# Optimization experiments

Measured on AMD Instinct MI355X. Metric: run time of the kernel, lower is better.

Reference implementation:

```python
import jax, jax.numpy as jnp
import numpy as np

BATCH, N_IN, N_OUT = 1024, 512, 512
GRID, DEGREE = 8, 3
NUM_BASIS = GRID + DEGREE  # 11
LO, HI = -3.0, 3.0
_h = (HI - LO) / GRID
# extended knot vector: GRID + 2*DEGREE + 1 knots -> GRID + DEGREE basis functions
KNOTS = jnp.asarray(np.linspace(LO - DEGREE * _h, HI + DEGREE * _h,
                                GRID + 2 * DEGREE + 1), dtype=jnp.float32)


def bspline_basis(x):
    """Cox-de Boor recursion. x: (batch, n_in) -> (batch, n_in, NUM_BASIS)."""
    t = KNOTS
    xb = x[..., None]
    B = ((xb >= t[:-1]) & (xb < t[1:])).astype(x.dtype)  # degree 0
    for d in range(1, DEGREE + 1):
        left = (xb - t[:-(d + 1)]) / (t[d:-1] - t[:-(d + 1)])
        right = (t[d + 1:] - xb) / (t[d + 1:] - t[1:-d])
        B = left * B[..., :-1] + right * B[..., 1:]
    return B


def setup_inputs() -> dict:
    key = jax.random.key(0)
    kx, kc, kw = jax.random.split(key, 3)
    x = jax.random.normal(kx, (BATCH, N_IN), dtype=jnp.float32)
    # xavier_normal_ init for c: fan_in = num_basis, fan_out = n_in*n_out
    c_std = float(np.sqrt(2.0 / (N_IN * N_OUT + NUM_BASIS)))
    c = jax.random.normal(kc, (N_IN * N_OUT, NUM_BASIS), dtype=jnp.float32) * c_std
    w_std = float(np.sqrt(2.0 / (N_IN + N_OUT)))
    w = jax.random.normal(kw, (N_IN, N_OUT), dtype=jnp.float32) * w_std
    return {"x": x, "c": c, "w": w}


def reference(x, c, w):
    # spline basis: (batch, n_in, K)
    bx = bspline_basis(x)
    # per-edge coefficients: (n_in, n_out, K)
    cr = c.reshape(N_IN, N_OUT, NUM_BASIS)
    # out[b,i,o] = sum_k bx[b,i,k] * c[i,o,k]
    spline = jnp.einsum('bik,iok->bio', bx, cr)
    # w * (silu(x) + spline), summed over n_in -> (batch, n_out)
    out = jnp.einsum('io,bio->bo', w, jax.nn.silu(x)[..., None] + spline)
    return out
```

## Files before the change

### kernel.cpp

```cpp
#include <hip/hip_runtime.h>

#define BATCH 1024
#define NIN   512
#define NOUT  512
#define NB    11
#define KSPLINE (NIN * NB)
#define KDIM    (KSPLINE + NIN)
#define SPLITS  8
#define BK      32

typedef short bf16x8 __attribute__((ext_vector_type(8)));
typedef float f32x4  __attribute__((ext_vector_type(4)));

__device__ __forceinline__ unsigned short f2bf(float f) {
  unsigned u = __float_as_uint(f);
  u += 0x7fff + ((u >> 16) & 1);
  return (unsigned short)(u >> 16);
}

__global__ __launch_bounds__(256) void k_basis(const float* __restrict__ x,
                                               unsigned short* __restrict__ A) {
  int tid = blockIdx.x * 256 + threadIdx.x;
  float xv = x[tid];
  float B[14];
#pragma unroll
  for (int j = 0; j < 14; ++j) {
    float t0 = -5.25f + 0.75f * (float)j;
    float t1 = t0 + 0.75f;
    B[j] = (xv >= t0 && xv < t1) ? 1.0f : 0.0f;
  }
#pragma unroll
  for (int d = 1; d <= 3; ++d) {
    float inv = 1.0f / (0.75f * (float)d);
#pragma unroll
    for (int j = 0; j <= 13 - d; ++j) {
      float tj   = -5.25f + 0.75f * (float)j;
      float tjd1 = tj + 0.75f * (float)(d + 1);
      B[j] = (xv - tj) * inv * B[j] + (tjd1 - xv) * inv * B[j + 1];
    }
  }
  int b = tid >> 9, i = tid & 511;
  unsigned short* row = A + (size_t)b * KDIM;
#pragma unroll
  for (int j = 0; j < NB; ++j) row[i * NB + j] = f2bf(B[j]);
  float sig = 1.0f / (1.0f + __expf(-xv));
  row[KSPLINE + i] = f2bf(xv * sig);
}

__global__ __launch_bounds__(256) void k_coef(const float* __restrict__ c,
                                              const float* __restrict__ w,
                                              unsigned short* __restrict__ Bt) {
  int o  = blockIdx.x;
  int kk = blockIdx.y * 256 + threadIdx.x;
  float v;
  if (kk < KSPLINE) {
    int i = kk / NB;
    int k = kk - i * NB;
    v = c[(size_t)(i * NOUT + o) * NB + k] * w[i * NOUT + o];
  } else {
    int i = kk - KSPLINE;
    v = w[i * NOUT + o];
  }
  Bt[(size_t)o * KDIM + kk] = f2bf(v);
}

__global__ __launch_bounds__(256) void k_gemm(const unsigned short* __restrict__ A,
                                              const unsigned short* __restrict__ Bt,
                                              float* __restrict__ out,
                                              int kchunk) {
  __shared__ unsigned short As[128 * BK];
  __shared__ unsigned short Bs[128 * BK];
  const int tid  = threadIdx.x;
  const int lane = tid & 63, wave = tid >> 6;
  const int wr = wave >> 1, wc = wave & 1;
  const int mbase = blockIdx.x * 128, nbase = blockIdx.y * 128;
  const int split = blockIdx.z;
  const int k0 = split * kchunk;

  f32x4 acc[4][4] = {};

  const int mrow = lane & 15;
  const int kq   = (lane >> 4) * 8;

  for (int kk = k0; kk < k0 + kchunk; kk += BK) {
#pragma unroll
    for (int it = 0; it < 2; ++it) {
      int ch  = it * 256 + tid;
      int row = ch >> 2, col = (ch & 3) * 8;
      const unsigned short* ga = A  + (size_t)(mbase + row) * KDIM + kk + col;
      const unsigned short* gb = Bt + (size_t)(nbase + row) * KDIM + kk + col;
      unsigned short* la = As + (it * 256 + wave * 64) * 8;
      unsigned short* lb = Bs + (it * 256 + wave * 64) * 8;
      __builtin_amdgcn_global_load_lds((__attribute__((address_space(1))) const void*)ga,
                                       (__attribute__((address_space(3))) void*)la, 16, 0, 0);
      __builtin_amdgcn_global_load_lds((__attribute__((address_space(1))) const void*)gb,
                                       (__attribute__((address_space(3))) void*)lb, 16, 0, 0);
    }
    __syncthreads();

    bf16x8 af[4], bfr[4];
#pragma unroll
    for (int mt = 0; mt < 4; ++mt)
      af[mt] = *(const bf16x8*)&As[(wr * 64 + mt * 16 + mrow) * BK + kq];
#pragma unroll
    for (int nt = 0; nt < 4; ++nt)
      bfr[nt] = *(const bf16x8*)&Bs[(wc * 64 + nt * 16 + mrow) * BK + kq];
#pragma unroll
    for (int mt = 0; mt < 4; ++mt)
#pragma unroll
      for (int nt = 0; nt < 4; ++nt)
        acc[mt][nt] = __builtin_amdgcn_mfma_f32_16x16x32_bf16(af[mt], bfr[nt], acc[mt][nt], 0, 0, 0);
    __syncthreads();
  }

  const int rq = (lane >> 4) * 4;
#pragma unroll
  for (int mt = 0; mt < 4; ++mt)
#pragma unroll
    for (int nt = 0; nt < 4; ++nt) {
      int colg = nbase + wc * 64 + nt * 16 + mrow;
#pragma unroll
      for (int r = 0; r < 4; ++r) {
        int rowg = mbase + wr * 64 + mt * 16 + rq + r;
        out[((size_t)split * BATCH + rowg) * NOUT + colg] = acc[mt][nt][r];
      }
    }
}

__global__ __launch_bounds__(256) void k_reduce(const float* __restrict__ part,
                                                float* __restrict__ out) {
  int t = blockIdx.x * 256 + threadIdx.x;
  f32x4 s = ((const f32x4*)part)[t];
#pragma unroll
  for (int sp = 1; sp < SPLITS; ++sp)
    s += ((const f32x4*)part)[(size_t)sp * (BATCH * NOUT / 4) + t];
  ((f32x4*)out)[t] = s;
}

extern "C" void kernel_launch(void* const* d_in, const int* in_sizes, int n_in,
                              void* d_out, int out_size, void* d_ws, size_t ws_size,
                              hipStream_t stream) {
  const float* x = (const float*)d_in[0];
  const float* c = (const float*)d_in[1];
  const float* w = (const float*)d_in[2];
  float* out = (float*)d_out;

  unsigned short* A  = (unsigned short*)d_ws;
  unsigned short* Bt = A + (size_t)BATCH * KDIM;
  float* part = (float*)((char*)d_ws + ((size_t)BATCH + NOUT) * KDIM * 2);

  size_t need = ((size_t)BATCH + NOUT) * KDIM * 2 + (size_t)SPLITS * BATCH * NOUT * 4;

  k_basis<<<dim3((BATCH * NIN) / 256), 256, 0, stream>>>(x, A);
  k_coef<<<dim3(NOUT, KDIM / 256), 256, 0, stream>>>(c, w, Bt);
  if (ws_size >= need) {
    k_gemm<<<dim3(8, 4, SPLITS), 256, 0, stream>>>(A, Bt, part, KDIM / SPLITS);
    k_reduce<<<dim3((BATCH * NOUT / 4) / 256), 256, 0, stream>>>(part, out);
  } else {
    k_gemm<<<dim3(8, 4, 1), 256, 0, stream>>>(A, Bt, out, KDIM);
  }
}
```

Baseline: 106.0 us.

## Fuse prep kernels, double GEMM K-tile with XOR-swizzled LDS, raise split-K to 16

Merges the basis and coefficient preparation kernels into one launch that branches on block index. In the GEMM, the K tile grows from 32 to 64 and LDS columns are XOR-swizzled by row so the wider fragment reads avoid bank conflicts. Split-K goes from 8 to 16 so 512 blocks fill the GPU instead of 256. The cost is twice as many fp32 partial buffers written and then read back by the reduce kernel, which adds memory traffic.

```diff
diff --git a/kernel.cpp b/kernel.cpp
--- a/kernel.cpp
+++ b/kernel.cpp
@@ -6,8 +6,9 @@
 #define NB    11
 #define KSPLINE (NIN * NB)
 #define KDIM    (KSPLINE + NIN)
-#define SPLITS  8
-#define BK      32
+#define SPLITS  16
+#define BK      64
+#define KCHUNK  (KDIM / SPLITS)
 
 typedef short bf16x8 __attribute__((ext_vector_type(8)));
 typedef float f32x4  __attribute__((ext_vector_type(4)));
@@ -18,50 +19,53 @@
   return (unsigned short)(u >> 16);
 }
 
-__global__ __launch_bounds__(256) void k_basis(const float* __restrict__ x,
-                                               unsigned short* __restrict__ A) {
-  int tid = blockIdx.x * 256 + threadIdx.x;
-  float xv = x[tid];
-  float B[14];
+__global__ __launch_bounds__(256) void k_prep(const float* __restrict__ x,
+                                              const float* __restrict__ c,
+                                              const float* __restrict__ w,
+                                              unsigned short* __restrict__ A,
+                                              unsigned short* __restrict__ Bt) {
+  int blk = blockIdx.x;
+  if (blk < 2048) {
+    int tid = blk * 256 + threadIdx.x;
+    float xv = x[tid];
+    float B[14];
 #pragma unroll
-  for (int j = 0; j < 14; ++j) {
-    float t0 = -5.25f + 0.75f * (float)j;
-    float t1 = t0 + 0.75f;
-    B[j] = (xv >= t0 && xv < t1) ? 1.0f : 0.0f;
+    for (int j = 0; j < 14; ++j) {
+      float t0 = -5.25f + 0.75f * (float)j;
+      float t1 = t0 + 0.75f;
+      B[j] = (xv >= t0 && xv < t1) ? 1.0f : 0.0f;
+    }
+#pragma unroll
+    for (int d = 1; d <= 3; ++d) {
+      float inv = 1.0f / (0.75f * (float)d);
+#pragma unroll
+      for (int j = 0; j <= 13 - d; ++j) {
+        float tj   = -5.25f + 0.75f * (float)j;
+        float tjd1 = tj + 0.75f * (float)(d + 1);
+        B[j] = (xv - tj) * inv * B[j] + (tjd1 - xv) * inv * B[j + 1];
+      }
+    }
+    int b = tid >> 9, i = tid & 511;
+    unsigned short* row = A + (size_t)b * KDIM;
+#pragma unroll
+    for (int j = 0; j < NB; ++j) row[i * NB + j] = f2bf(B[j]);
+    float sig = 1.0f / (1.0f + __expf(-xv));
+    row[KSPLINE + i] = f2bf(xv * sig);
+  } else {
+    int bc = blk - 2048;
+    int o  = bc & 511;
+    int kk = (bc >> 9) * 256 + threadIdx.x;
+    float v;
+    if (kk < KSPLINE) {
+      int i = kk / NB;
+      int k = kk - i * NB;
+      v = c[(size_t)i * KSPLINE + o * NB + k] * w[i * NOUT + o];
+    } else {
+      int i = kk - KSPLINE;
+      v = w[i * NOUT + o];
+    }
+    Bt[(size_t)o * KDIM + kk] = f2bf(v);
   }
-#pragma unroll
-  for (int d = 1; d <= 3; ++d) {
-    float inv = 1.0f / (0.75f * (float)d);
-#pragma unroll
-    for (int j = 0; j <= 13 - d; ++j) {
-      float tj   = -5.25f + 0.75f * (float)j;
-      float tjd1 = tj + 0.75f * (float)(d + 1);
-      B[j] = (xv - tj) * inv * B[j] + (tjd1 - xv) * inv * B[j + 1];
-    }
-  }
-  int b = tid >> 9, i = tid & 511;
-  unsigned short* row = A + (size_t)b * KDIM;
-#pragma unroll
-  for (int j = 0; j < NB; ++j) row[i * NB + j] = f2bf(B[j]);
-  float sig = 1.0f / (1.0f + __expf(-xv));
-  row[KSPLINE + i] = f2bf(xv * sig);
-}
-
-__global__ __launch_bounds__(256) void k_coef(const float* __restrict__ c,
-                                              const float* __restrict__ w,
-                                              unsigned short* __restrict__ Bt) {
-  int o  = blockIdx.x;
-  int kk = blockIdx.y * 256 + threadIdx.x;
-  float v;
-  if (kk < KSPLINE) {
-    int i = kk / NB;
-    int k = kk - i * NB;
-    v = c[(size_t)(i * NOUT + o) * NB + k] * w[i * NOUT + o];
-  } else {
-    int i = kk - KSPLINE;
-    v = w[i * NOUT + o];
-  }
-  Bt[(size_t)o * KDIM + kk] = f2bf(v);
 }
 
 __global__ __launch_bounds__(256) void k_gemm(const unsigned short* __restrict__ A,
@@ -81,12 +85,15 @@
 
   const int mrow = lane & 15;
   const int kq   = (lane >> 4) * 8;
+  const int swz  = mrow & 7;
 
   for (int kk = k0; kk < k0 + kchunk; kk += BK) {
 #pragma unroll
-    for (int it = 0; it < 2; ++it) {
+    for (int it = 0; it < 4; ++it) {
       int ch  = it * 256 + tid;
-      int row = ch >> 2, col = (ch & 3) * 8;
+      int row = ch >> 3;
+      int cgl = ch & 7;
+      int col = (cgl ^ (row & 7)) * 8;
       const unsigned short* ga = A  + (size_t)(mbase + row) * KDIM + kk + col;
       const unsigned short* gb = Bt + (size_t)(nbase + row) * KDIM + kk + col;
       unsigned short* la = As + (it * 256 + wave * 64) * 8;
@@ -98,18 +105,27 @@
     }
     __syncthreads();
 
-    bf16x8 af[4], bfr[4];
 #pragma unroll
-    for (int mt = 0; mt < 4; ++mt)
-      af[mt] = *(const bf16x8*)&As[(wr * 64 + mt * 16 + mrow) * BK + kq];
+    for (int ks = 0; ks < BK; ks += 32) {
+      bf16x8 af[4], bfr[4];
 #pragma unroll
-    for (int nt = 0; nt < 4; ++nt)
-      bfr[nt] = *(const bf16x8*)&Bs[(wc * 64 + nt * 16 + mrow) * BK + kq];
+      for (int mt = 0; mt < 4; ++mt) {
+        int row = wr * 64 + mt * 16 + mrow;
+        int cg  = ((ks + kq) >> 3) ^ swz;
+        af[mt] = *(const bf16x8*)&As[row * BK + cg * 8];
+      }
 #pragma unroll
-    for (int mt = 0; mt < 4; ++mt)
+      for (int nt = 0; nt < 4; ++nt) {
+        int row = wc * 64 + nt * 16 + mrow;
+        int cg  = ((ks + kq) >> 3) ^ swz;
+        bfr[nt] = *(const bf16x8*)&Bs[row * BK + cg * 8];
+      }
 #pragma unroll
-      for (int nt = 0; nt < 4; ++nt)
-        acc[mt][nt] = __builtin_amdgcn_mfma_f32_16x16x32_bf16(af[mt], bfr[nt], acc[mt][nt], 0, 0, 0);
+      for (int mt = 0; mt < 4; ++mt)
+#pragma unroll
+        for (int nt = 0; nt < 4; ++nt)
+          acc[mt][nt] = __builtin_amdgcn_mfma_f32_16x16x32_bf16(af[mt], bfr[nt], acc[mt][nt], 0, 0, 0);
+    }
     __syncthreads();
   }
 
@@ -151,10 +167,9 @@
 
   size_t need = ((size_t)BATCH + NOUT) * KDIM * 2 + (size_t)SPLITS * BATCH * NOUT * 4;
 
-  k_basis<<<dim3((BATCH * NIN) / 256), 256, 0, stream>>>(x, A);
-  k_coef<<<dim3(NOUT, KDIM / 256), 256, 0, stream>>>(c, w, Bt);
+  k_prep<<<dim3(2048 + 512 * (KDIM / 256)), 256, 0, stream>>>(x, c, w, A, Bt);
   if (ws_size >= need) {
-    k_gemm<<<dim3(8, 4, SPLITS), 256, 0, stream>>>(A, Bt, part, KDIM / SPLITS);
+    k_gemm<<<dim3(8, 4, SPLITS), 256, 0, stream>>>(A, Bt, part, KCHUNK);
     k_reduce<<<dim3((BATCH * NOUT / 4) / 256), 256, 0, stream>>>(part, out);
   } else {
     k_gemm<<<dim3(8, 4, 1), 256, 0, stream>>>(A, Bt, out, KDIM);
```

Measured after the change: 99.38 us. 6.3% less time.
